# Optimization experiments

Hardware: AMD Instinct MI355X
Metric: run time of the kernel (lower is better)

Reference implementation:

```python
import jax, jax.numpy as jnp
import numpy as np

EPS = 1e-5

def setup_inputs() -> dict:
    key = jax.random.key(0)
    ks = jax.random.split(key, 6)
    B, S, F, D = 512, 64, 768, 256
    # xavier-ish scales for weights
    return {
        "audio_feat": jax.random.normal(ks[0], (B, S, F), dtype=jnp.float32),
        "visual_feat": jax.random.normal(ks[1], (B, S, F), dtype=jnp.float32),
        "Wa": jax.random.normal(ks[2], (F, D), dtype=jnp.float32) * (1.0 / np.sqrt(F)),
        "ba": jnp.zeros((D,), dtype=jnp.float32),
        "Wv": jax.random.normal(ks[3], (F, D), dtype=jnp.float32) * (1.0 / np.sqrt(F)),
        "bv": jnp.zeros((D,), dtype=jnp.float32),
        "corr": jax.random.normal(ks[4], (D, D), dtype=jnp.float32) * float(np.sqrt(2.0 / (D + D))),
        "Wb": jax.random.normal(ks[5], (2 * D, 64), dtype=jnp.float32) * (1.0 / np.sqrt(2 * D)),
        "bb": jnp.zeros((64,), dtype=jnp.float32),
        "gamma": jnp.ones((64,), dtype=jnp.float32),
        "beta": jnp.zeros((64,), dtype=jnp.float32),
    }


def reference(audio_feat, visual_feat, Wa, ba, Wv, bv, corr, Wb, bb, gamma, beta):
    # project: [b,s,768] -> [b,s,256]
    a = jnp.einsum('bsf,fd->bsd', audio_feat, Wa) + ba      # audio proj
    v = jnp.einsum('bsf,fd->bsd', visual_feat, Wv) + bv     # vision proj
    vT = jnp.swapaxes(v, 1, 2)                              # [b,d,s]
    # bilinear correlation: cc[b,i,j] = a[b,i,:] @ corr @ v[b,j,:]
    cc = jnp.einsum('bid,de,bje->bij', a, corr, v)          # [b,sa,sv]
    audio_att = jax.nn.softmax(cc, axis=1)                  # softmax over audio positions
    visual_att = jax.nn.softmax(cc, axis=2)                 # softmax over visual positions (of cc^T along dim 1)
    # attended features, both [b,d,s]
    att_a = jnp.einsum('bid,bij->bdj', a, audio_att) + jnp.swapaxes(a, 1, 2)
    att_v = jnp.einsum('bdj,bij->bdi', vT, jnp.swapaxes(visual_att, 1, 2))
    # note: bmm(vT [b,d,sv], visual_att^T' ...) -> torch does vT @ visual_att_t where
    # visual_att_t[b,j,i] = visual_att[b,i,j]; equivalent einsum below
    att_v = jnp.einsum('bdj,bji->bdi', vT, jnp.swapaxes(visual_att, 1, 2)) + vT
    fused = jnp.concatenate([att_a, att_v], axis=1)         # [b,2d,s]
    fused = jnp.swapaxes(fused, 1, 2)                       # [b,s,2d]
    h = jnp.einsum('bsk,ko->bso', fused, Wb) + bb           # [b,s,64]
    mu = jnp.mean(h, axis=-1, keepdims=True)
    var = jnp.mean(jnp.square(h - mu), axis=-1, keepdims=True)
    h = (h - mu) * jax.lax.rsqrt(var + EPS) * gamma + beta
    return jax.nn.relu(h)
```

## Files before the change

kernel.cpp:

```cpp
#include <hip/hip_runtime.h>

typedef _Float16 f16x8 __attribute__((ext_vector_type(8)));
typedef _Float16 f16x4 __attribute__((ext_vector_type(4)));
typedef float    f32x4 __attribute__((ext_vector_type(4)));

#define A16_OFF   0u
#define V16_OFF   16777216u
#define WAP_OFF   33554432u
#define WVP_OFF   33947648u
#define CORRT_OFF 34340864u
#define WBT_OFF   34471936u

__device__ __forceinline__ void gl_lds16(const void* g, void* l) {
    __builtin_amdgcn_global_load_lds(
        (const __attribute__((address_space(1))) void*)g,
        (__attribute__((address_space(3))) void*)l, 16, 0, 0);
}
#define SBAR()   __builtin_amdgcn_s_barrier()
#define SCHED0() __builtin_amdgcn_sched_barrier(0)

__global__ __launch_bounds__(256) void k_pack(
    const float* __restrict__ Wa, const float* __restrict__ Wv,
    _Float16* __restrict__ WaP, _Float16* __restrict__ WvP)
{
    int bid = blockIdx.x;
    int z = bid >= 96;
    int b = z ? bid - 96 : bid;
    const float* W = z ? Wv : Wa;
    _Float16* P = z ? WvP : WaP;
    int c = b * 256 + threadIdx.x;
    int col = c & 255, q = (c >> 8) & 3, ks = c >> 10;
    int k0 = ks * 32 + q * 8;
    _Float16 tmp[8];
    #pragma unroll
    for (int e = 0; e < 8; ++e)
        tmp[e] = (_Float16)W[(size_t)(k0 + e) * 256 + col];
    *reinterpret_cast<f16x8*>(P + (size_t)c * 8) = *reinterpret_cast<const f16x8*>(tmp);
}

__global__ __launch_bounds__(256) void k_tr(
    const float* __restrict__ corr, const float* __restrict__ Wb,
    _Float16* __restrict__ corrT, _Float16* __restrict__ WbT)
{
    __shared__ _Float16 tile[64][72];
    int bid = blockIdx.x;
    const float* src; _Float16* dst; int R, C, tr, tc;
    if (bid < 16) { src = corr; dst = corrT; R = 256; C = 256; tr = bid >> 2; tc = bid & 3; }
    else          { src = Wb;   dst = WbT;   R = 512; C = 64;  tr = bid - 16; tc = 0;       }
    int r0 = tr * 64, c0 = tc * 64;
    int t = threadIdx.x;
    #pragma unroll
    for (int it = 0; it < 16; ++it) {
        int idx = t + it * 256;
        int r = idx >> 6, c = idx & 63;
        tile[r][c] = (_Float16)src[(size_t)(r0 + r) * C + (c0 + c)];
    }
    __syncthreads();
    #pragma unroll
    for (int it = 0; it < 16; ++it) {
        int idx = t + it * 256;
        int c = idx >> 6, r = idx & 63;
        dst[(size_t)(c0 + c) * R + (r0 + r)] = tile[r][c];
    }
}

__global__ __launch_bounds__(256, 2) void k_proj(
    const float* __restrict__ Xa, const float* __restrict__ Xv,
    const _Float16* __restrict__ WaP, const _Float16* __restrict__ WvP,
    const float* __restrict__ ba, const float* __restrict__ bv,
    _Float16* __restrict__ Aout, _Float16* __restrict__ Vout)
{
    __shared__ __align__(16) char Abuf[2][16384];
    __shared__ __align__(16) char Bbuf[2][16384];

    const int bid = blockIdx.x;
    const int z = bid >> 8, mb = bid & 255;
    const float*    X    = z ? Xv  : Xa;
    const _Float16* WP   = z ? WvP : WaP;
    const float*    bias = z ? bv  : ba;
    _Float16*       Out  = z ? Vout : Aout;
    const int m0 = mb * 128;

    const int t = threadIdx.x, lane = t & 63, w = t >> 6;
    const int wr = w >> 1, wc = w & 1;
    const int q = lane >> 4, lm = lane & 15;

    f32x4 acc[4][8] = {};

    auto stageA = [&](int ks, int buf) {
        #pragma unroll
        for (int it = 0; it < 4; ++it) {
            int idx = t + it * 256;
            int r = idx >> 3, c = idx & 7;
            int gc = c ^ (r & 7);
            char* l = Abuf[buf] + (it * 256 + w * 64) * 16;
            gl_lds16(X + (size_t)(m0 + r) * 768 + ks * 32 + gc * 4, l);
        }
    };
    auto stageB = [&](int ks, int buf) {
        #pragma unroll
        for (int it = 0; it < 4; ++it) {
            int idx = t + it * 256;
            char* l = Bbuf[buf] + (it * 256 + w * 64) * 16;
            gl_lds16(WP + ((size_t)ks * 1024 + idx) * 8, l);
        }
    };

    stageA(0, 0); stageB(0, 0);
    stageA(1, 1); stageB(1, 1);
    asm volatile("s_waitcnt vmcnt(8)" ::: "memory"); SCHED0();
    SBAR();

    for (int ks = 0; ks < 24; ++ks) {
        const int cur = ks & 1;
        f16x8 af[4], bf[8];
        #pragma unroll
        for (int mf = 0; mf < 4; ++mf) {
            int r = wr * 64 + mf * 16 + lm;
            const char* base = Abuf[cur] + r * 128;
            int c0 = (2 * q) ^ (r & 7);
            int c1 = (2 * q + 1) ^ (r & 7);
            f32x4 lo = *reinterpret_cast<const f32x4*>(base + c0 * 16);
            f32x4 hi = *reinterpret_cast<const f32x4*>(base + c1 * 16);
            f16x4 l4 = __builtin_convertvector(lo, f16x4);
            f16x4 h4 = __builtin_convertvector(hi, f16x4);
            af[mf] = __builtin_shufflevector(l4, h4, 0, 1, 2, 3, 4, 5, 6, 7);
        }
        #pragma unroll
        for (int nf = 0; nf < 8; ++nf) {
            int col = wc * 128 + nf * 16 + lm;
            bf[nf] = *reinterpret_cast<const f16x8*>(Bbuf[cur] + (q * 256 + col) * 16);
        }
        asm volatile("s_waitcnt lgkmcnt(0)" ::: "memory"); SCHED0();
        SBAR();
        if (ks + 2 < 24) { stageA(ks + 2, cur); stageB(ks + 2, cur); }
        __builtin_amdgcn_s_setprio(1);
        #pragma unroll
        for (int nf = 0; nf < 8; ++nf)
            #pragma unroll
            for (int mf = 0; mf < 4; ++mf)
                acc[mf][nf] = __builtin_amdgcn_mfma_f32_16x16x32_f16(af[mf], bf[nf], acc[mf][nf], 0, 0, 0);
        __builtin_amdgcn_s_setprio(0);
        if (ks < 22) { asm volatile("s_waitcnt vmcnt(8)" ::: "memory"); }
        else         { asm volatile("s_waitcnt vmcnt(0)" ::: "memory"); }
        SCHED0();
        SBAR();
    }

    float biasv[8];
    #pragma unroll
    for (int nf = 0; nf < 8; ++nf)
        biasv[nf] = bias[wc * 128 + nf * 16 + lm];

    _Float16* Cs = (_Float16*)Abuf;
    #pragma unroll
    for (int mf = 0; mf < 4; ++mf)
        #pragma unroll
        for (int nf = 0; nf < 8; ++nf)
            #pragma unroll
            for (int r = 0; r < 4; ++r)
                Cs[(wr * 64 + mf * 16 + q * 4 + r) * 256 + wc * 128 + nf * 16 + lm] =
                    (_Float16)(acc[mf][nf][r] + biasv[nf]);
    __syncthreads();
    #pragma unroll
    for (int it = 0; it < 16; ++it) {
        int idx = t + it * 256;
        int row = idx >> 5, c = idx & 31;
        f16x8 vv = *reinterpret_cast<const f16x8*>(Cs + row * 256 + c * 8);
        *reinterpret_cast<f16x8*>(Out + (size_t)(m0 + row) * 256 + c * 8) = vv;
    }
}

#define SM_A    0u
#define SM_V    33792u
#define SM_AC   67584u
#define SM_CC   101376u
#define SM_ATA  118272u
#define SM_ATV  127488u
#define SM_AWT  136704u
#define SM_VWT  145920u
#define SM_RED  155136u
#define SM_TOTAL 159232u

__global__ __launch_bounds__(256) void k_fuse(
    const _Float16* __restrict__ A16, const _Float16* __restrict__ V16,
    const _Float16* __restrict__ corrT, const _Float16* __restrict__ WbT,
    const float* __restrict__ bb, const float* __restrict__ gamma,
    const float* __restrict__ beta, float* __restrict__ out)
{
    extern __shared__ char sm[];
    _Float16* a_s   = (_Float16*)(sm + SM_A);
    _Float16* v_s   = (_Float16*)(sm + SM_V);
    _Float16* ac_s  = (_Float16*)(sm + SM_AC);
    float*    cc_s  = (float*)(sm + SM_CC);
    _Float16* attAT = (_Float16*)(sm + SM_ATA);
    _Float16* attV  = (_Float16*)(sm + SM_ATV);
    _Float16* awT   = (_Float16*)(sm + SM_AWT);
    _Float16* vwT   = (_Float16*)(sm + SM_VWT);
    float*    red   = (float*)(sm + SM_RED);

    const int b = blockIdx.x;
    const int t = threadIdx.x, lane = t & 63, w = t >> 6;
    const int q = lane >> 4, lm = lane & 15;

    const _Float16* Ab = A16 + (size_t)b * 64 * 256;
    const _Float16* Vb = V16 + (size_t)b * 64 * 256;
    #pragma unroll
    for (int it = 0; it < 8; ++it) {
        int idx = t + it * 256;
        int row = idx >> 5, kc = idx & 31;
        *reinterpret_cast<f16x8*>(a_s + row * 264 + kc * 8) =
            *reinterpret_cast<const f16x8*>(Ab + row * 256 + kc * 8);
        *reinterpret_cast<f16x8*>(v_s + row * 264 + kc * 8) =
            *reinterpret_cast<const f16x8*>(Vb + row * 256 + kc * 8);
    }
    __syncthreads();

    {
        f32x4 acc[4][4] = {};
        for (int ks = 0; ks < 8; ++ks) {
            f16x8 af[4];
            #pragma unroll
            for (int mf = 0; mf < 4; ++mf)
                af[mf] = *reinterpret_cast<const f16x8*>(a_s + (mf * 16 + lm) * 264 + ks * 32 + q * 8);
            #pragma unroll
            for (int nf = 0; nf < 4; ++nf) {
                int e = w * 64 + nf * 16 + lm;
                f16x8 bf = *reinterpret_cast<const f16x8*>(corrT + (size_t)e * 256 + ks * 32 + q * 8);
                #pragma unroll
                for (int mf = 0; mf < 4; ++mf)
                    acc[mf][nf] = __builtin_amdgcn_mfma_f32_16x16x32_f16(af[mf], bf, acc[mf][nf], 0, 0, 0);
            }
        }
        #pragma unroll
        for (int mf = 0; mf < 4; ++mf)
            #pragma unroll
            for (int nf = 0; nf < 4; ++nf)
                #pragma unroll
                for (int r = 0; r < 4; ++r)
                    ac_s[(mf * 16 + 4 * q + r) * 264 + (w * 64 + nf * 16 + lm)] = (_Float16)acc[mf][nf][r];
    }
    __syncthreads();

    {
        f32x4 acc[4] = {};
        for (int ks = 0; ks < 8; ++ks) {
            f16x8 bf = *reinterpret_cast<const f16x8*>(v_s + (w * 16 + lm) * 264 + ks * 32 + q * 8);
            #pragma unroll
            for (int mf = 0; mf < 4; ++mf) {
                f16x8 af = *reinterpret_cast<const f16x8*>(ac_s + (mf * 16 + lm) * 264 + ks * 32 + q * 8);
                acc[mf] = __builtin_amdgcn_mfma_f32_16x16x32_f16(af, bf, acc[mf], 0, 0, 0);
            }
        }
        #pragma unroll
        for (int mf = 0; mf < 4; ++mf)
            #pragma unroll
            for (int r = 0; r < 4; ++r)
                cc_s[(mf * 16 + 4 * q + r) * 66 + (w * 16 + lm)] = acc[mf][r];
    }
    __syncthreads();

    {
        int j = t & 63, seg = w;
        float cmx = -1e30f, rmx = -1e30f;
        #pragma unroll
        for (int k = 0; k < 16; ++k) {
            int i = seg * 16 + k;
            cmx = fmaxf(cmx, cc_s[i * 66 + j]);
            rmx = fmaxf(rmx, cc_s[j * 66 + i]);
        }
        red[0 * 256 + seg * 64 + j] = cmx;
        red[2 * 256 + seg * 64 + j] = rmx;
        __syncthreads();
        float cm = fmaxf(fmaxf(red[0 * 256 + 0 * 64 + j], red[0 * 256 + 1 * 64 + j]),
                         fmaxf(red[0 * 256 + 2 * 64 + j], red[0 * 256 + 3 * 64 + j]));
        float rm = fmaxf(fmaxf(red[2 * 256 + 0 * 64 + j], red[2 * 256 + 1 * 64 + j]),
                         fmaxf(red[2 * 256 + 2 * 64 + j], red[2 * 256 + 3 * 64 + j]));
        float cs = 0.f, rs = 0.f;
        #pragma unroll
        for (int k = 0; k < 16; ++k) {
            int i = seg * 16 + k;
            cs += __expf(cc_s[i * 66 + j] - cm);
            rs += __expf(cc_s[j * 66 + i] - rm);
        }
        red[1 * 256 + seg * 64 + j] = cs;
        red[3 * 256 + seg * 64 + j] = rs;
        __syncthreads();
        float csum = red[1 * 256 + 0 * 64 + j] + red[1 * 256 + 1 * 64 + j] +
                     red[1 * 256 + 2 * 64 + j] + red[1 * 256 + 3 * 64 + j];
        float rsum = red[3 * 256 + 0 * 64 + j] + red[3 * 256 + 1 * 64 + j] +
                     red[3 * 256 + 2 * 64 + j] + red[3 * 256 + 3 * 64 + j];
        float cinv = 1.f / csum, rinv = 1.f / rsum;
        #pragma unroll
        for (int k = 0; k < 16; ++k) {
            int i = seg * 16 + k;
            float pa = __expf(cc_s[i * 66 + j] - cm) * cinv;
            if (i == j) pa += 1.f;
            attAT[j * 72 + i] = (_Float16)pa;
            float pv = __expf(cc_s[j * 66 + i] - rm) * rinv;
            if (i == j) pv += 1.f;
            attV[j * 72 + i] = (_Float16)pv;
        }
    }

    {
        int isV = w >> 1, wcol = w & 1;
        const _Float16* src = isV ? v_s : a_s;
        const int doff = isV ? 256 : 0;
        f32x4 acc[4][2] = {};
        for (int ks = 0; ks < 8; ++ks) {
            f16x8 af[4];
            #pragma unroll
            for (int mf = 0; mf < 4; ++mf)
                af[mf] = *reinterpret_cast<const f16x8*>(src + (mf * 16 + lm) * 264 + ks * 32 + q * 8);
            #pragma unroll
            for (int nf = 0; nf < 2; ++nf) {
                int o = wcol * 32 + nf * 16 + lm;
                f16x8 bf = *reinterpret_cast<const f16x8*>(WbT + (size_t)o * 512 + doff + ks * 32 + q * 8);
                #pragma unroll
                for (int mf = 0; mf < 4; ++mf)
                    acc[mf][nf] = __builtin_amdgcn_mfma_f32_16x16x32_f16(af[mf], bf, acc[mf][nf], 0, 0, 0);
            }
        }
        _Float16* dst = isV ? vwT : awT;
        #pragma unroll
        for (int mf = 0; mf < 4; ++mf)
            #pragma unroll
            for (int nf = 0; nf < 2; ++nf)
                #pragma unroll
                for (int r = 0; r < 4; ++r)
                    dst[(wcol * 32 + nf * 16 + lm) * 72 + (mf * 16 + 4 * q + r)] = (_Float16)acc[mf][nf][r];
    }
    __syncthreads();

    f32x4 hacc[4] = {};
    #pragma unroll
    for (int kk = 0; kk < 2; ++kk) {
        f16x8 a1 = *reinterpret_cast<const f16x8*>(attAT + (16 * w + lm) * 72 + kk * 32 + q * 8);
        f16x8 a2 = *reinterpret_cast<const f16x8*>(attV  + (16 * w + lm) * 72 + kk * 32 + q * 8);
        #pragma unroll
        for (int nf = 0; nf < 4; ++nf) {
            f16x8 b1 = *reinterpret_cast<const f16x8*>(awT + (nf * 16 + lm) * 72 + kk * 32 + q * 8);
            f16x8 b2 = *reinterpret_cast<const f16x8*>(vwT + (nf * 16 + lm) * 72 + kk * 32 + q * 8);
            hacc[nf] = __builtin_amdgcn_mfma_f32_16x16x32_f16(a1, b1, hacc[nf], 0, 0, 0);
            hacc[nf] = __builtin_amdgcn_mfma_f32_16x16x32_f16(a2, b2, hacc[nf], 0, 0, 0);
        }
    }

    {
        float bbv[4], gv[4], bev[4];
        #pragma unroll
        for (int nf = 0; nf < 4; ++nf) {
            int o = nf * 16 + lm;
            bbv[nf] = bb[o]; gv[nf] = gamma[o]; bev[nf] = beta[o];
        }
        #pragma unroll
        for (int r = 0; r < 4; ++r) {
            float vals[4]; float s1 = 0.f, s2 = 0.f;
            #pragma unroll
            for (int nf = 0; nf < 4; ++nf) {
                float hv = hacc[nf][r] + bbv[nf];
                vals[nf] = hv; s1 += hv; s2 += hv * hv;
            }
            #pragma unroll
            for (int m = 1; m < 16; m <<= 1) {
                s1 += __shfl_xor(s1, m, 64);
                s2 += __shfl_xor(s2, m, 64);
            }
            float mu = s1 * 0.015625f;
            float var = s2 * 0.015625f - mu * mu;
            float rstd = rsqrtf(var + 1e-5f);
            int s = 16 * w + 4 * q + r;
            float* orow = out + ((size_t)b * 64 + s) * 64;
            #pragma unroll
            for (int nf = 0; nf < 4; ++nf) {
                float y = (vals[nf] - mu) * rstd * gv[nf] + bev[nf];
                orow[nf * 16 + lm] = fmaxf(y, 0.f);
            }
        }
    }
}

extern "C" void kernel_launch(void* const* d_in, const int* in_sizes, int n_in,
                              void* d_out, int out_size, void* d_ws, size_t ws_size,
                              hipStream_t stream) {
    const float* Xa    = (const float*)d_in[0];
    const float* Xv    = (const float*)d_in[1];
    const float* Wa    = (const float*)d_in[2];
    const float* ba    = (const float*)d_in[3];
    const float* Wv    = (const float*)d_in[4];
    const float* bv    = (const float*)d_in[5];
    const float* corr  = (const float*)d_in[6];
    const float* Wb    = (const float*)d_in[7];
    const float* bb    = (const float*)d_in[8];
    const float* gamma = (const float*)d_in[9];
    const float* beta  = (const float*)d_in[10];
    float* out = (float*)d_out;
    char* ws = (char*)d_ws;

    _Float16* a16   = (_Float16*)(ws + A16_OFF);
    _Float16* v16   = (_Float16*)(ws + V16_OFF);
    _Float16* WaP   = (_Float16*)(ws + WAP_OFF);
    _Float16* WvP   = (_Float16*)(ws + WVP_OFF);
    _Float16* corrT = (_Float16*)(ws + CORRT_OFF);
    _Float16* WbT   = (_Float16*)(ws + WBT_OFF);

    hipLaunchKernelGGL(k_pack, dim3(192), dim3(256), 0, stream,
                       Wa, Wv, WaP, WvP);
    hipLaunchKernelGGL(k_tr, dim3(24), dim3(256), 0, stream,
                       corr, Wb, corrT, WbT);
    hipLaunchKernelGGL(k_proj, dim3(512), dim3(256), 0, stream,
                       Xa, Xv, WaP, WvP, ba, bv, a16, v16);
    (void)hipFuncSetAttribute((const void*)k_fuse,
                              hipFuncAttributeMaxDynamicSharedMemorySize, SM_TOTAL);
    hipLaunchKernelGGL(k_fuse, dim3(512), dim3(256), SM_TOTAL, stream,
                       a16, v16, corrT, WbT, bb, gamma, beta, out);
}
```

Measured before the change: 86.87 us.

## Merge weight prep kernels and widen projection GEMM to 8 waves per block

Combines the two weight-preparation kernels into one launch, removing a kernel launch. The projection GEMM moves from 4 to 8 waves per 128-row block, so each wave owns 32 rows instead of 64. Its accumulator footprint halves and the launch bounds target more resident waves. The packed weight layout changes to fragment-major so each lane reads its B fragment with one contiguous load, and MFMAs are interleaved with the B loads. The trade-off is less A/B reuse per wave and more barrier participants per block.

```diff
diff --git a/kernel.cpp b/kernel.cpp
--- a/kernel.cpp
+++ b/kernel.cpp
@@ -11,67 +11,70 @@
 #define CORRT_OFF 34340864u
 #define WBT_OFF   34471936u
 
+#define SCHED0() __builtin_amdgcn_sched_barrier(0)
+#define SBAR()   __builtin_amdgcn_s_barrier()
+
 __device__ __forceinline__ void gl_lds16(const void* g, void* l) {
     __builtin_amdgcn_global_load_lds(
         (const __attribute__((address_space(1))) void*)g,
         (__attribute__((address_space(3))) void*)l, 16, 0, 0);
 }
-#define SBAR()   __builtin_amdgcn_s_barrier()
-#define SCHED0() __builtin_amdgcn_sched_barrier(0)
-
-__global__ __launch_bounds__(256) void k_pack(
+
+__global__ __launch_bounds__(256) void k_prep(
     const float* __restrict__ Wa, const float* __restrict__ Wv,
-    _Float16* __restrict__ WaP, _Float16* __restrict__ WvP)
-{
-    int bid = blockIdx.x;
-    int z = bid >= 96;
-    int b = z ? bid - 96 : bid;
-    const float* W = z ? Wv : Wa;
-    _Float16* P = z ? WvP : WaP;
-    int c = b * 256 + threadIdx.x;
-    int col = c & 255, q = (c >> 8) & 3, ks = c >> 10;
-    int k0 = ks * 32 + q * 8;
-    _Float16 tmp[8];
-    #pragma unroll
-    for (int e = 0; e < 8; ++e)
-        tmp[e] = (_Float16)W[(size_t)(k0 + e) * 256 + col];
-    *reinterpret_cast<f16x8*>(P + (size_t)c * 8) = *reinterpret_cast<const f16x8*>(tmp);
-}
-
-__global__ __launch_bounds__(256) void k_tr(
     const float* __restrict__ corr, const float* __restrict__ Wb,
+    _Float16* __restrict__ WaP, _Float16* __restrict__ WvP,
     _Float16* __restrict__ corrT, _Float16* __restrict__ WbT)
 {
     __shared__ _Float16 tile[64][72];
     int bid = blockIdx.x;
-    const float* src; _Float16* dst; int R, C, tr, tc;
-    if (bid < 16) { src = corr; dst = corrT; R = 256; C = 256; tr = bid >> 2; tc = bid & 3; }
-    else          { src = Wb;   dst = WbT;   R = 512; C = 64;  tr = bid - 16; tc = 0;       }
-    int r0 = tr * 64, c0 = tc * 64;
     int t = threadIdx.x;
-    #pragma unroll
-    for (int it = 0; it < 16; ++it) {
-        int idx = t + it * 256;
-        int r = idx >> 6, c = idx & 63;
-        tile[r][c] = (_Float16)src[(size_t)(r0 + r) * C + (c0 + c)];
-    }
-    __syncthreads();
-    #pragma unroll
-    for (int it = 0; it < 16; ++it) {
-        int idx = t + it * 256;
-        int c = idx >> 6, r = idx & 63;
-        dst[(size_t)(c0 + c) * R + (r0 + r)] = tile[r][c];
+    if (bid < 192) {
+        int z = bid >= 96;
+        int b = z ? bid - 96 : bid;
+        const float* W = z ? Wv : Wa;
+        _Float16* P = z ? WvP : WaP;
+        int kc = b >> 2, nbg = b & 3;
+        int l = t & 63, sub = t >> 6;
+        int nb = nbg * 4 + sub;
+        int q = l >> 4, lm = l & 15;
+        int k0 = kc * 32 + q * 8;
+        int n = nb * 16 + lm;
+        _Float16 tmp[8];
+        #pragma unroll
+        for (int e = 0; e < 8; ++e)
+            tmp[e] = (_Float16)W[(size_t)(k0 + e) * 256 + n];
+        *reinterpret_cast<f16x8*>(P + ((size_t)(kc * 16 + nb) * 64 + l) * 8) =
+            *reinterpret_cast<const f16x8*>(tmp);
+    } else {
+        int b2 = bid - 192;
+        const float* src; _Float16* dst; int R, C, tr, tc;
+        if (b2 < 16) { src = corr; dst = corrT; R = 256; C = 256; tr = b2 >> 2; tc = b2 & 3; }
+        else         { src = Wb;   dst = WbT;   R = 512; C = 64;  tr = b2 - 16; tc = 0;      }
+        int r0 = tr * 64, c0 = tc * 64;
+        #pragma unroll
+        for (int it = 0; it < 16; ++it) {
+            int idx = t + it * 256;
+            int r = idx >> 6, c = idx & 63;
+            tile[r][c] = (_Float16)src[(size_t)(r0 + r) * C + (c0 + c)];
+        }
+        __syncthreads();
+        #pragma unroll
+        for (int it = 0; it < 16; ++it) {
+            int idx = t + it * 256;
+            int c = idx >> 6, r = idx & 63;
+            dst[(size_t)(c0 + c) * R + (r0 + r)] = tile[r][c];
+        }
     }
 }
 
-__global__ __launch_bounds__(256, 2) void k_proj(
+__global__ __launch_bounds__(512, 4) void k_proj(
     const float* __restrict__ Xa, const float* __restrict__ Xv,
     const _Float16* __restrict__ WaP, const _Float16* __restrict__ WvP,
     const float* __restrict__ ba, const float* __restrict__ bv,
     _Float16* __restrict__ Aout, _Float16* __restrict__ Vout)
 {
-    __shared__ __align__(16) char Abuf[2][16384];
-    __shared__ __align__(16) char Bbuf[2][16384];
+    __shared__ __align__(16) char smem[65536];
 
     const int bid = blockIdx.x;
     const int z = bid >> 8, mb = bid & 255;
@@ -85,39 +88,44 @@
     const int wr = w >> 1, wc = w & 1;
     const int q = lane >> 4, lm = lane & 15;
 
-    f32x4 acc[4][8] = {};
+    f32x4 acc[2][8] = {};
 
     auto stageA = [&](int ks, int buf) {
-        #pragma unroll
-        for (int it = 0; it < 4; ++it) {
-            int idx = t + it * 256;
+        char* base = smem + buf * 16384;
+        #pragma unroll
+        for (int it = 0; it < 2; ++it) {
+            int idx = t + it * 512;
             int r = idx >> 3, c = idx & 7;
             int gc = c ^ (r & 7);
-            char* l = Abuf[buf] + (it * 256 + w * 64) * 16;
+            char* l = base + (it * 512 + w * 64) * 16;
             gl_lds16(X + (size_t)(m0 + r) * 768 + ks * 32 + gc * 4, l);
         }
     };
     auto stageB = [&](int ks, int buf) {
-        #pragma unroll
-        for (int it = 0; it < 4; ++it) {
-            int idx = t + it * 256;
-            char* l = Bbuf[buf] + (it * 256 + w * 64) * 16;
+        char* base = smem + 32768 + buf * 16384;
+        #pragma unroll
+        for (int it = 0; it < 2; ++it) {
+            int idx = t + it * 512;
+            char* l = base + (it * 512 + w * 64) * 16;
             gl_lds16(WP + ((size_t)ks * 1024 + idx) * 8, l);
         }
     };
 
     stageA(0, 0); stageB(0, 0);
     stageA(1, 1); stageB(1, 1);
-    asm volatile("s_waitcnt vmcnt(8)" ::: "memory"); SCHED0();
+    asm volatile("s_waitcnt vmcnt(4)" ::: "memory"); SCHED0();
     SBAR();
 
     for (int ks = 0; ks < 24; ++ks) {
         const int cur = ks & 1;
-        f16x8 af[4], bf[8];
-        #pragma unroll
-        for (int mf = 0; mf < 4; ++mf) {
-            int r = wr * 64 + mf * 16 + lm;
-            const char* base = Abuf[cur] + r * 128;
+        const char* Ac = smem + cur * 16384;
+        const char* Bc = smem + 32768 + cur * 16384;
+
+        f16x8 af[2];
+        #pragma unroll
+        for (int mf = 0; mf < 2; ++mf) {
+            int r = wr * 32 + mf * 16 + lm;
+            const char* base = Ac + r * 128;
             int c0 = (2 * q) ^ (r & 7);
             int c1 = (2 * q + 1) ^ (r & 7);
             f32x4 lo = *reinterpret_cast<const f32x4*>(base + c0 * 16);
@@ -128,20 +136,15 @@
         }
         #pragma unroll
         for (int nf = 0; nf < 8; ++nf) {
-            int col = wc * 128 + nf * 16 + lm;
-            bf[nf] = *reinterpret_cast<const f16x8*>(Bbuf[cur] + (q * 256 + col) * 16);
+            int nb = wc * 8 + nf;
+            f16x8 bf = *reinterpret_cast<const f16x8*>(Bc + (nb * 64 + lane) * 16);
+            acc[0][nf] = __builtin_amdgcn_mfma_f32_16x16x32_f16(af[0], bf, acc[0][nf], 0, 0, 0);
+            acc[1][nf] = __builtin_amdgcn_mfma_f32_16x16x32_f16(af[1], bf, acc[1][nf], 0, 0, 0);
         }
         asm volatile("s_waitcnt lgkmcnt(0)" ::: "memory"); SCHED0();
         SBAR();
         if (ks + 2 < 24) { stageA(ks + 2, cur); stageB(ks + 2, cur); }
-        __builtin_amdgcn_s_setprio(1);
-        #pragma unroll
-        for (int nf = 0; nf < 8; ++nf)
-            #pragma unroll
-            for (int mf = 0; mf < 4; ++mf)
-                acc[mf][nf] = __builtin_amdgcn_mfma_f32_16x16x32_f16(af[mf], bf[nf], acc[mf][nf], 0, 0, 0);
-        __builtin_amdgcn_s_setprio(0);
-        if (ks < 22) { asm volatile("s_waitcnt vmcnt(8)" ::: "memory"); }
+        if (ks < 22) { asm volatile("s_waitcnt vmcnt(4)" ::: "memory"); }
         else         { asm volatile("s_waitcnt vmcnt(0)" ::: "memory"); }
         SCHED0();
         SBAR();
@@ -152,19 +155,19 @@
     for (int nf = 0; nf < 8; ++nf)
         biasv[nf] = bias[wc * 128 + nf * 16 + lm];
 
-    _Float16* Cs = (_Float16*)Abuf;
+    _Float16* Cs = (_Float16*)smem;
     #pragma unroll
-    for (int mf = 0; mf < 4; ++mf)
+    for (int mf = 0; mf < 2; ++mf)
         #pragma unroll
         for (int nf = 0; nf < 8; ++nf)
             #pragma unroll
             for (int r = 0; r < 4; ++r)
-                Cs[(wr * 64 + mf * 16 + q * 4 + r) * 256 + wc * 128 + nf * 16 + lm] =
+                Cs[(wr * 32 + mf * 16 + q * 4 + r) * 256 + wc * 128 + nf * 16 + lm] =
                     (_Float16)(acc[mf][nf][r] + biasv[nf]);
     __syncthreads();
     #pragma unroll
-    for (int it = 0; it < 16; ++it) {
-        int idx = t + it * 256;
+    for (int it = 0; it < 8; ++it) {
+        int idx = t + it * 512;
         int row = idx >> 5, c = idx & 31;
         f16x8 vv = *reinterpret_cast<const f16x8*>(Cs + row * 256 + c * 8);
         *reinterpret_cast<f16x8*>(Out + (size_t)(m0 + row) * 256 + c * 8) = vv;
@@ -405,11 +408,9 @@
     _Float16* corrT = (_Float16*)(ws + CORRT_OFF);
     _Float16* WbT   = (_Float16*)(ws + WBT_OFF);
 
-    hipLaunchKernelGGL(k_pack, dim3(192), dim3(256), 0, stream,
-                       Wa, Wv, WaP, WvP);
-    hipLaunchKernelGGL(k_tr, dim3(24), dim3(256), 0, stream,
-                       corr, Wb, corrT, WbT);
-    hipLaunchKernelGGL(k_proj, dim3(512), dim3(256), 0, stream,
+    hipLaunchKernelGGL(k_prep, dim3(216), dim3(256), 0, stream,
+                       Wa, Wv, corr, Wb, WaP, WvP, corrT, WbT);
+    hipLaunchKernelGGL(k_proj, dim3(512), dim3(512), 0, stream,
                        Xa, Xv, WaP, WvP, ba, bv, a16, v16);
     (void)hipFuncSetAttribute((const void*)k_fuse,
                               hipFuncAttributeMaxDynamicSharedMemorySize, SM_TOTAL);
```

New measurement: 87.29 us. No clear change (+0.5%).
